# Kernel optimization log

Hardware: AMD Instinct MI355X
Metric: run time of the kernel (lower is better)

Reference implementation:

```python
import jax, jax.numpy as jnp
import numpy as np

B, T, D = 4, 2048, 1024
H = 16
DK = D // H
SCALE = 1.0 / np.sqrt(DK)
EPS_LN = 1e-5
EPS_NORM = 1e-8


def setup_inputs() -> dict:
    key = jax.random.key(0)
    ks = jax.random.split(key, 12)
    gain = 1.0 / np.sqrt(2.0)
    # xavier_uniform bound for square [D, D] weight with gain
    bound = gain * np.sqrt(6.0 / (D + D))

    def w(k):
        return jax.random.uniform(k, (D, D), jnp.float32, -bound, bound)

    return {
        "x": jax.random.normal(ks[0], (B, T, D), jnp.float32),
        "mask": jax.random.bernoulli(ks[1], 0.1, (B, T)),  # True = masked out
        "wq": w(ks[2]), "bq": jnp.zeros((D,), jnp.float32),
        "wk": w(ks[3]), "bk": jnp.zeros((D,), jnp.float32),
        "wv": w(ks[4]), "bv": jnp.zeros((D,), jnp.float32),
        "wo": w(ks[5]), "bo": jnp.zeros((D,), jnp.float32),
        "ln_g": jnp.ones((D,), jnp.float32),
        "ln_b": jnp.zeros((D,), jnp.float32),
    }


def _layernorm(x, g, b):
    mu = jnp.mean(x, axis=-1, keepdims=True)
    var = jnp.var(x, axis=-1, keepdims=True)
    return (x - mu) * jax.lax.rsqrt(var + EPS_LN) * g + b


def _l2norm(x):
    # torch F.normalize: x / clamp_min(||x||_2, eps)
    n = jnp.sqrt(jnp.sum(x * x, axis=-1, keepdims=True))
    return x / jnp.maximum(n, EPS_NORM)


def reference(x, mask, wq, bq, wk, bk, wv, bv, wo, bo, ln_g, ln_b):
    xn = _layernorm(x, ln_g, ln_b)  # q_norm applied to shared input

    def proj(w, bias):
        y = jnp.einsum("btd,ed->bte", xn, w) + bias
        return y.reshape(B, T, H, DK).transpose(0, 2, 1, 3)  # [B,H,T,DK]

    Q = _l2norm(proj(wq, bq))
    K = _l2norm(proj(wk, bk))
    V = proj(wv, bv)

    scores = jnp.einsum("bhqd,bhkd->bhqk", Q, K) * SCALE
    scores = jnp.clip(scores, -10.0, 10.0)
    scores = jnp.where(mask[:, None, None, :], -10000.0, scores)
    scores = scores - jnp.max(scores, axis=-1, keepdims=True)
    attn = jax.nn.softmax(scores, axis=-1)

    out = jnp.einsum("bhqk,bhkd->bhqd", attn, V)
    out = out.transpose(0, 2, 1, 3).reshape(B, T, D)
    out = jnp.einsum("btd,ed->bte", out, wo) + bo
    return out * 0.5
```

## Files before the change

### kernel.cpp

```cpp
#include <hip/hip_runtime.h>
#include <hip/hip_bf16.h>
#include <cstdint>
#include <cstddef>
#include <cstring>

typedef unsigned short u16;
typedef unsigned char u8;
typedef __attribute__((ext_vector_type(8))) short short8;
typedef __attribute__((ext_vector_type(4))) float f32x4;

#define B_    4
#define T_    2048
#define D_    1024
#define H_    16
#define DK_   64
#define QSCALE_ 0.18033688011112042f

__device__ __forceinline__ float bf2f(u16 u) {
    unsigned int x = ((unsigned int)u) << 16;
    float f; __builtin_memcpy(&f, &x, 4); return f;
}
__device__ __forceinline__ u16 f2bf(float f) {
    unsigned int x; __builtin_memcpy(&x, &f, 4);
    x += 0x7fffu + ((x >> 16) & 1u);
    return (u16)(x >> 16);
}
__device__ __forceinline__ unsigned pack_bf16_hu(float lo, float hi) {
    unsigned a, b;
    __builtin_memcpy(&a, &lo, 4);
    __builtin_memcpy(&b, &hi, 4);
    return __builtin_amdgcn_perm(b + 0x8000u, a + 0x8000u, 0x07060302u);
}

__device__ __forceinline__ int sniff_flag(const u16* __restrict__ x, int tid) {
    __shared__ int sc[4];
    int cnt = 0;
    for (int i = tid; i < 512; i += 256) {
        int e = (x[8 * i] >> 7) & 0xFF;
        if (e > 137 || (e >= 1 && e < 97)) cnt++;
    }
    for (int o = 1; o < 64; o <<= 1) cnt += __shfl_xor(cnt, o);
    if ((tid & 63) == 0) sc[tid >> 6] = cnt;
    __syncthreads();
    return (sc[0] + sc[1] + sc[2] + sc[3] > 128) ? 1 : 0;
}

__global__ __launch_bounds__(256) void mega_prep(
    const u16* __restrict__ x, const u8* __restrict__ m,
    const void* wq, const void* wk, const void* wv, const void* wo,
    const void* bq, const void* bk, const void* bv, const void* bo,
    const void* lng, const void* lnb,
    u16* __restrict__ wqc, u16* __restrict__ wkc,
    u16* __restrict__ wvc, u16* __restrict__ woc,
    u16* __restrict__ vecs, float* __restrict__ msk, int* flag,
    u16* __restrict__ xn)
{
    int tid = threadIdx.x;
    int f = sniff_flag(x, tid);
    int id = blockIdx.x;

    if (id < 4096) {
        int mat = id >> 10;
        const void* s = (mat == 0) ? wq : (mat == 1) ? wk : (mat == 2) ? wv : wo;
        u16* d = (mat == 0) ? wqc : (mat == 1) ? wkc : (mat == 2) ? wvc : woc;
        int i4 = (id & 1023) * 256 + tid;
        if (f) {
            float4 v = ((const float4*)s)[i4];
            ushort4 o; o.x = f2bf(v.x); o.y = f2bf(v.y); o.z = f2bf(v.z); o.w = f2bf(v.w);
            ((ushort4*)d)[i4] = o;
        } else {
            ((ushort4*)d)[i4] = ((const ushort4*)s)[i4];
        }
    } else if (id < 12288) {
        __shared__ float rs[4], rq[4];
        int row = id - 4096;
        int t = tid;
        float v[4];
        if (f) {
            float4 f4 = ((const float4*)x)[(size_t)row * 256 + t];
            v[0] = f4.x; v[1] = f4.y; v[2] = f4.z; v[3] = f4.w;
        } else {
            ushort4 uv = ((const ushort4*)x)[(size_t)row * 256 + t];
            v[0] = bf2f(uv.x); v[1] = bf2f(uv.y); v[2] = bf2f(uv.z); v[3] = bf2f(uv.w);
        }
        float s = v[0] + v[1] + v[2] + v[3];
        float q = v[0]*v[0] + v[1]*v[1] + v[2]*v[2] + v[3]*v[3];
        for (int o = 1; o < 64; o <<= 1) { s += __shfl_xor(s, o); q += __shfl_xor(q, o); }
        int wv_ = t >> 6, ln = t & 63;
        if (ln == 0) { rs[wv_] = s; rq[wv_] = q; }
        __syncthreads();
        s = rs[0] + rs[1] + rs[2] + rs[3];
        q = rq[0] + rq[1] + rq[2] + rq[3];
        float mu   = s * (1.0f / D_);
        float var  = q * (1.0f / D_) - mu * mu;
        float rstd = rsqrtf(var + 1e-5f);
        u16 o4[4];
        for (int i = 0; i < 4; i++) {
            float gv, bv_;
            if (f) { gv = ((const float*)lng)[t*4 + i]; bv_ = ((const float*)lnb)[t*4 + i]; }
            else   { gv = bf2f(((const u16*)lng)[t*4 + i]); bv_ = bf2f(((const u16*)lnb)[t*4 + i]); }
            o4[i] = f2bf((v[i] - mu) * rstd * gv + bv_);
        }
        ushort4 ov; ov.x = o4[0]; ov.y = o4[1]; ov.z = o4[2]; ov.w = o4[3];
        *(ushort4*)(xn + (size_t)row * D_ + t * 4) = ov;
    } else {
        __shared__ int sb[4];
        int k = id - 12288;
        int bits = 0;
        for (int i = tid; i < B_ * T_; i += 256)
            if (m[i]) bits |= (i & 7);
        for (int o = 1; o < 64; o <<= 1) bits |= __shfl_xor(bits, o);
        if ((tid & 63) == 0) sb[tid >> 6] = bits;
        __syncthreads();
        bits = sb[0] | sb[1] | sb[2] | sb[3];
        int stride = (bits & 1) ? 1 : (bits & 2) ? 2 : (bits & 4) ? 4 : 8;
        for (int i = tid; i < 1024; i += 256) {
            int idx = k * 1024 + i;
            msk[idx] = m[(size_t)idx * stride] ? -200.f : 0.f;
        }
        if (k == 0) {
            if (tid == 0) *flag = f;
            const void* ss[6] = {bq, bk, bv, bo, lng, lnb};
            for (int t = 0; t < 6; t++) {
                const void* s = ss[t];
                for (int i = tid; i < 1024; i += 256)
                    vecs[t * 1024 + i] = f ? f2bf(((const float*)s)[i]) : ((const u16*)s)[i];
            }
        }
    }
}

__global__ __launch_bounds__(256) void gemm_bt(
    const u16* __restrict__ A,
    const u16* __restrict__ W0, const u16* __restrict__ W1, const u16* __restrict__ W2,
    const u16* __restrict__ bias_all, int bias_idx0,
    u16* __restrict__ C0, u16* __restrict__ C1, u16* __restrict__ C2,
    float scale, const int* __restrict__ flag, int use_flag, int qkv_mode)
{
    const int K = 1024, N = 1024;
    const u16* W; const u16* bias; u16* C;
    if (blockIdx.z == 0)      { W = W0; bias = bias_all + (size_t)bias_idx0 * 1024;       C = C0; }
    else if (blockIdx.z == 1) { W = W1; bias = bias_all + (size_t)(bias_idx0 + 1) * 1024; C = C1; }
    else                      { W = W2; bias = bias_all + (size_t)(bias_idx0 + 2) * 1024; C = C2; }

    __shared__ u16 As[128 * 32];
    __shared__ u16 Bs[128 * 32];

    int tid  = threadIdx.x;
    int wave = tid >> 6, lane = tid & 63;
    int wm = wave >> 1, wn = wave & 1;
    int quad = lane >> 4, l16 = lane & 15;
    int bm = blockIdx.x * 128, bn = blockIdx.y * 128;

    f32x4 acc[4][4];
    const f32x4 fz = {0.f, 0.f, 0.f, 0.f};
    for (int i = 0; i < 4; i++) for (int j = 0; j < 4; j++) acc[i][j] = fz;

    int srow = lane >> 2;
    int scol = (lane & 3) * 8;
    const u16* gA0 = A + (size_t)(bm + wave * 32 + srow) * K + scol;
    const u16* gB0 = W + (size_t)(bn + wave * 32 + srow) * K + scol;

    for (int k0 = 0; k0 < K; k0 += 32) {
        for (int i = 0; i < 2; i++) {
            __builtin_amdgcn_global_load_lds(
                (const __attribute__((address_space(1))) void*)(gA0 + (size_t)i * 16 * K + k0),
                (__attribute__((address_space(3))) void*)(As + (wave * 32 + i * 16) * 32),
                16, 0, 0);
            __builtin_amdgcn_global_load_lds(
                (const __attribute__((address_space(1))) void*)(gB0 + (size_t)i * 16 * K + k0),
                (__attribute__((address_space(3))) void*)(Bs + (wave * 32 + i * 16) * 32),
                16, 0, 0);
        }
        __syncthreads();
        short8 a[4], b[4];
        for (int i = 0; i < 4; i++)
            a[i] = *(const short8*)(As + (wm * 64 + i * 16 + l16) * 32 + quad * 8);
        for (int j = 0; j < 4; j++)
            b[j] = *(const short8*)(Bs + (wn * 64 + j * 16 + l16) * 32 + quad * 8);
        for (int i = 0; i < 4; i++)
            for (int j = 0; j < 4; j++)
                acc[i][j] = __builtin_amdgcn_mfma_f32_16x16x32_bf16(a[i], b[j], acc[i][j], 0, 0, 0);
        __syncthreads();
    }

    if (qkv_mode) {
        if (blockIdx.z == 2) {
            for (int j = 0; j < 4; j++) {
                int col = bn + wn * 64 + j * 16 + l16;
                int h = col >> 6, d = col & 63;
                float bi = bf2f(bias[col]);
                for (int i = 0; i < 4; i++) {
                    int row0 = bm + wm * 64 + i * 16 + quad * 4;
                    int bq = row0 >> 11, t0 = row0 & 2047;
                    ushort4 pk;
                    pk.x = f2bf(acc[i][j][0] + bi); pk.y = f2bf(acc[i][j][1] + bi);
                    pk.z = f2bf(acc[i][j][2] + bi); pk.w = f2bf(acc[i][j][3] + bi);
                    *(ushort4*)(C + ((size_t)((bq * 16 + h) * 64 + d)) * 2048 + t0) = pk;
                }
            }
        } else {
            float sc2 = (blockIdx.z == 0) ? QSCALE_ : 1.0f;
            float bi[4];
            for (int j = 0; j < 4; j++) bi[j] = bf2f(bias[bn + wn * 64 + j * 16 + l16]);
            for (int i = 0; i < 4; i++) {
                int row0 = bm + wm * 64 + i * 16 + quad * 4;
                for (int r = 0; r < 4; r++) {
                    float v[4]; float s = 0.f;
                    for (int j = 0; j < 4; j++) { v[j] = acc[i][j][r] + bi[j]; s += v[j] * v[j]; }
                    s += __shfl_xor(s, 1); s += __shfl_xor(s, 2);
                    s += __shfl_xor(s, 4); s += __shfl_xor(s, 8);
                    float scl = sc2 / fmaxf(sqrtf(s), 1e-8f);
                    for (int j = 0; j < 4; j++) {
                        int col = bn + wn * 64 + j * 16 + l16;
                        C[(size_t)(row0 + r) * N + col] = f2bf(v[j] * scl);
                    }
                }
            }
        }
        return;
    }

    int f32out = use_flag ? *flag : 0;
    for (int j = 0; j < 4; j++) {
        int col = bn + wn * 64 + j * 16 + l16;
        float bi = bf2f(bias[col]);
        for (int i = 0; i < 4; i++) {
            int row0 = bm + wm * 64 + i * 16 + quad * 4;
            for (int r = 0; r < 4; r++) {
                float o = (acc[i][j][r] + bi) * scale;
                if (f32out) ((float*)C)[(size_t)(row0 + r) * N + col] = o;
                else        C[(size_t)(row0 + r) * N + col] = f2bf(o);
            }
        }
    }
}

__global__ __launch_bounds__(256, 4) void attn_kernel(
    const u16* __restrict__ Q, const u16* __restrict__ Kg,
    const u16* __restrict__ Vt, const float* __restrict__ msk,
    u16* __restrict__ Oout)
{
    __shared__ __align__(16) u16 Ks[2 * 64 * 64];
    __shared__ __align__(16) u16 VTs[2 * 64 * 64];

    int tid  = threadIdx.x;
    int wave = tid >> 6, lane = tid & 63;
    int quad = lane >> 4, l16 = lane & 15;
    int q0 = blockIdx.y * 128;
    int b  = blockIdx.x >> 4, h = blockIdx.x & 15;
    const size_t base  = (size_t)b * T_ * D_ + h * DK_;
    const size_t vbase = (size_t)((b * 16 + h) * 64) * T_;

    short8 qa[2][2];
    for (int g = 0; g < 2; g++) {
        const u16* qrow = Q + base + (size_t)(q0 + wave * 32 + g * 16 + l16) * D_;
        qa[g][0] = *(const short8*)(qrow + quad * 8);
        qa[g][1] = *(const short8*)(qrow + 32 + quad * 8);
    }

    const float* mq = msk + b * T_ + quad * 8;

    int rL0 = wave * 8 + (lane >> 3);
    int rL1 = rL0 + 32;
    int c   = lane & 7;
    int k0i = (rL0 & 32) + ((rL0 >> 2) & 3) * 8 + ((rL0 >> 4) & 1) * 4 + (rL0 & 3);
    int k1i = (rL1 & 32) + ((rL1 >> 2) & 3) * 8 + ((rL1 >> 4) & 1) * 4 + (rL1 & 3);
    const u16* kgs0 = Kg + base + (size_t)k0i * D_ + (c ^ (rL0 & 7)) * 8;
    const u16* kgs1 = Kg + base + (size_t)k1i * D_ + (c ^ (rL1 & 7)) * 8;
    const u16* vgs0 = Vt + vbase + (size_t)rL0 * T_ + (c ^ (rL0 & 7)) * 8;
    const u16* vgs1 = Vt + vbase + (size_t)rL1 * T_ + (c ^ (rL1 & 7)) * 8;
    u16* kd0 = Ks  + (wave * 8) * 64;
    u16* kd1 = Ks  + (wave * 8 + 32) * 64;
    u16* vd0 = VTs + (wave * 8) * 64;
    u16* vd1 = VTs + (wave * 8 + 32) * 64;

#define STAGE(BUF, KOFF) do {                                                   \
    __builtin_amdgcn_global_load_lds(                                           \
        (const __attribute__((address_space(1))) void*)(kgs0 + (size_t)(KOFF) * D_), \
        (__attribute__((address_space(3))) void*)(kd0 + (BUF) * 4096), 16, 0, 0); \
    __builtin_amdgcn_global_load_lds(                                           \
        (const __attribute__((address_space(1))) void*)(kgs1 + (size_t)(KOFF) * D_), \
        (__attribute__((address_space(3))) void*)(kd1 + (BUF) * 4096), 16, 0, 0); \
    __builtin_amdgcn_global_load_lds(                                           \
        (const __attribute__((address_space(1))) void*)(vgs0 + (KOFF)),         \
        (__attribute__((address_space(3))) void*)(vd0 + (BUF) * 4096), 16, 0, 0); \
    __builtin_amdgcn_global_load_lds(                                           \
        (const __attribute__((address_space(1))) void*)(vgs1 + (KOFF)),         \
        (__attribute__((address_space(3))) void*)(vd1 + (BUF) * 4096), 16, 0, 0); \
} while (0)

    STAGE(0, 0);
    __syncthreads();

    const u16* kr_lo = Ks + l16 * 64 + ((quad ^ (l16 & 7)) * 8);
    const u16* kr_hi = Ks + l16 * 64 + (((4 + quad) ^ (l16 & 7)) * 8);
    const u16* vr0 = VTs + l16 * 64 + ((quad ^ (l16 & 7)) * 8);
    const u16* vr1 = VTs + l16 * 64 + (((4 + quad) ^ (l16 & 7)) * 8);

    f32x4 o_acc[2][4];
    for (int g = 0; g < 2; g++) for (int j = 0; j < 4; j++) o_acc[g][j] = f32x4{0.f, 0.f, 0.f, 0.f};
    float rowsum[2] = {0.f, 0.f};

#define TILE_BODY(CUR, NXT, KT) do {                                            \
    int ktn = ((KT) + 64) & (T_ - 1);                                           \
    STAGE(NXT, ktn);                                                            \
    f32x4 pmt[2][2];                                                            \
    for (int j2 = 0; j2 < 2; j2++)                                              \
        for (int s = 0; s < 2; s++)                                             \
            pmt[j2][s] = *(const f32x4*)(mq + (KT) + j2 * 32 + s * 4);          \
    __builtin_amdgcn_s_setprio(1);                                              \
    for (int j2 = 0; j2 < 2; j2++) {                                            \
        unsigned pw[2][4];                                                      \
        for (int s = 0; s < 2; s++) {                                           \
            short8 kb0 = *(const short8*)(kr_lo + (CUR) * 4096 + (j2 * 32 + s * 16) * 64); \
            short8 kb1 = *(const short8*)(kr_hi + (CUR) * 4096 + (j2 * 32 + s * 16) * 64); \
            for (int g = 0; g < 2; g++) {                                       \
                f32x4 s4 = __builtin_amdgcn_mfma_f32_16x16x32_bf16(kb0, qa[g][0], pmt[j2][s], 0, 0, 0); \
                s4       = __builtin_amdgcn_mfma_f32_16x16x32_bf16(kb1, qa[g][1], s4, 0, 0, 0); \
                float p0 = __builtin_exp2f(s4[0]);                              \
                float p1 = __builtin_exp2f(s4[1]);                              \
                float p2 = __builtin_exp2f(s4[2]);                              \
                float p3 = __builtin_exp2f(s4[3]);                              \
                rowsum[g] += (p0 + p1) + (p2 + p3);                             \
                pw[g][s * 2]     = pack_bf16_hu(p0, p1);                        \
                pw[g][s * 2 + 1] = pack_bf16_hu(p2, p3);                        \
            }                                                                   \
        }                                                                       \
        short8 pb[2];                                                           \
        __builtin_memcpy(&pb[0], &pw[0][0], 16);                                \
        __builtin_memcpy(&pb[1], &pw[1][0], 16);                                \
        const u16* vr = (j2 ? vr1 : vr0) + (CUR) * 4096;                        \
        for (int jd = 0; jd < 4; jd++) {                                        \
            short8 vv = *(const short8*)(vr + jd * 16 * 64);                    \
            o_acc[0][jd] = __builtin_amdgcn_mfma_f32_16x16x32_bf16(vv, pb[0], o_acc[0][jd], 0, 0, 0); \
            o_acc[1][jd] = __builtin_amdgcn_mfma_f32_16x16x32_bf16(vv, pb[1], o_acc[1][jd], 0, 0, 0); \
        }                                                                       \
    }                                                                           \
    __builtin_amdgcn_s_setprio(0);                                              \
    __syncthreads();                                                            \
} while (0)

    for (int kt = 0; kt < T_; kt += 128) {
        TILE_BODY(0, 1, kt);
        TILE_BODY(1, 0, kt + 64);
    }
#undef TILE_BODY
#undef STAGE

    for (int g = 0; g < 2; g++) {
        float l = rowsum[g];
        l += __shfl_xor(l, 16);
        l += __shfl_xor(l, 32);
        float inv = 1.0f / fmaxf(l, 1e-20f);
        size_t orow = base + (size_t)(q0 + wave * 32 + g * 16 + l16) * D_;
        for (int jd = 0; jd < 4; jd++) {
            ushort4 pk;
            pk.x = f2bf(o_acc[g][jd][0] * inv);
            pk.y = f2bf(o_acc[g][jd][1] * inv);
            pk.z = f2bf(o_acc[g][jd][2] * inv);
            pk.w = f2bf(o_acc[g][jd][3] * inv);
            *(ushort4*)(Oout + orow + jd * 16 + quad * 4) = pk;
        }
    }
}

extern "C" void kernel_launch(void* const* d_in, const int* in_sizes, int n_in,
                              void* d_out, int out_size, void* d_ws, size_t ws_size,
                              hipStream_t stream)
{
    const void* x    = d_in[0];
    const u8*   mask = (const u8*)d_in[1];
    const void* wq   = d_in[2];
    const void* bq   = d_in[3];
    const void* wk   = d_in[4];
    const void* bk   = d_in[5];
    const void* wv   = d_in[6];
    const void* bv   = d_in[7];
    const void* wo   = d_in[8];
    const void* bo   = d_in[9];
    const void* lng  = d_in[10];
    const void* lnb  = d_in[11];

    const size_t NTOK = (size_t)B_ * T_;
    u16* xn  = (u16*)d_ws;
    u16* Kb  = xn + NTOK * D_;
    u16* Vtb = Kb + NTOK * D_;
    u16* wqc = Vtb + NTOK * D_;
    u16* wkc = wqc + (size_t)D_ * D_;
    u16* wvc = wkc + (size_t)D_ * D_;
    u16* woc = wvc + (size_t)D_ * D_;
    u16* vecs = woc + (size_t)D_ * D_;
    float* msk = (float*)(vecs + 6 * 1024);
    int* flag = (int*)(msk + 8192);
    u16* Qb  = (u16*)d_out;

    mega_prep<<<dim3(12296), 256, 0, stream>>>(
        (const u16*)x, mask, wq, wk, wv, wo, bq, bk, bv, bo, lng, lnb,
        wqc, wkc, wvc, woc, vecs, msk, flag, xn);
    gemm_bt<<<dim3(64, 8, 3), 256, 0, stream>>>(xn, wqc, wkc, wvc, vecs, 0, Qb, Kb, Vtb, 1.0f, flag, 0, 1);
    attn_kernel<<<dim3(64, 16), 256, 0, stream>>>(Qb, Kb, Vtb, msk, xn);
    gemm_bt<<<dim3(64, 8, 1), 256, 0, stream>>>(xn, woc, woc, woc, vecs, 3, (u16*)d_out, (u16*)d_out, (u16*)d_out, 0.5f, flag, 1, 0);
}
```

Baseline: 344.7 us.

## Swap GEMM MFMA operands for row-contiguous stores; compute attention rowsum via MFMA

In the GEMM kernel, the MFMA operands are swapped for the Q/K and output projections, so each lane holds four consecutive columns of one row. This allows vectorized ushort4/float4 stores and a two-shuffle L2-norm reduction, replacing strided scalar stores and a four-shuffle reduction. In the attention kernel, the per-row softmax denominator is now accumulated with an extra MFMA against a vector of bf16 ones instead of scalar VALU adds and final shuffles. This adds two MFMAs per sub-tile and sums the bf16-rounded probabilities, which matches the values fed to P·V.

```diff
diff --git a/kernel.cpp b/kernel.cpp
--- a/kernel.cpp
+++ b/kernel.cpp
@@ -152,6 +152,8 @@
     int quad = lane >> 4, l16 = lane & 15;
     int bm = blockIdx.x * 128, bn = blockIdx.y * 128;
 
+    int do_swap = !(qkv_mode && blockIdx.z == 2);
+
     f32x4 acc[4][4];
     const f32x4 fz = {0.f, 0.f, 0.f, 0.f};
     for (int i = 0; i < 4; i++) for (int j = 0; j < 4; j++) acc[i][j] = fz;
@@ -178,59 +180,81 @@
             a[i] = *(const short8*)(As + (wm * 64 + i * 16 + l16) * 32 + quad * 8);
         for (int j = 0; j < 4; j++)
             b[j] = *(const short8*)(Bs + (wn * 64 + j * 16 + l16) * 32 + quad * 8);
-        for (int i = 0; i < 4; i++)
-            for (int j = 0; j < 4; j++)
-                acc[i][j] = __builtin_amdgcn_mfma_f32_16x16x32_bf16(a[i], b[j], acc[i][j], 0, 0, 0);
+        if (do_swap) {
+            for (int i = 0; i < 4; i++)
+                for (int j = 0; j < 4; j++)
+                    acc[i][j] = __builtin_amdgcn_mfma_f32_16x16x32_bf16(b[j], a[i], acc[i][j], 0, 0, 0);
+        } else {
+            for (int i = 0; i < 4; i++)
+                for (int j = 0; j < 4; j++)
+                    acc[i][j] = __builtin_amdgcn_mfma_f32_16x16x32_bf16(a[i], b[j], acc[i][j], 0, 0, 0);
+        }
         __syncthreads();
     }
 
-    if (qkv_mode) {
-        if (blockIdx.z == 2) {
-            for (int j = 0; j < 4; j++) {
-                int col = bn + wn * 64 + j * 16 + l16;
-                int h = col >> 6, d = col & 63;
-                float bi = bf2f(bias[col]);
-                for (int i = 0; i < 4; i++) {
-                    int row0 = bm + wm * 64 + i * 16 + quad * 4;
-                    int bq = row0 >> 11, t0 = row0 & 2047;
-                    ushort4 pk;
-                    pk.x = f2bf(acc[i][j][0] + bi); pk.y = f2bf(acc[i][j][1] + bi);
-                    pk.z = f2bf(acc[i][j][2] + bi); pk.w = f2bf(acc[i][j][3] + bi);
-                    *(ushort4*)(C + ((size_t)((bq * 16 + h) * 64 + d)) * 2048 + t0) = pk;
-                }
-            }
-        } else {
-            float sc2 = (blockIdx.z == 0) ? QSCALE_ : 1.0f;
-            float bi[4];
-            for (int j = 0; j < 4; j++) bi[j] = bf2f(bias[bn + wn * 64 + j * 16 + l16]);
+    if (qkv_mode && blockIdx.z == 2) {
+        for (int j = 0; j < 4; j++) {
+            int col = bn + wn * 64 + j * 16 + l16;
+            int h = col >> 6, d = col & 63;
+            float bi = bf2f(bias[col]);
             for (int i = 0; i < 4; i++) {
                 int row0 = bm + wm * 64 + i * 16 + quad * 4;
+                int bq = row0 >> 11, t0 = row0 & 2047;
+                ushort4 pk;
+                pk.x = f2bf(acc[i][j][0] + bi); pk.y = f2bf(acc[i][j][1] + bi);
+                pk.z = f2bf(acc[i][j][2] + bi); pk.w = f2bf(acc[i][j][3] + bi);
+                *(ushort4*)(C + ((size_t)((bq * 16 + h) * 64 + d)) * 2048 + t0) = pk;
+            }
+        }
+        return;
+    }
+
+    float bi[4][4];
+    for (int j = 0; j < 4; j++) {
+        ushort4 b4 = *(const ushort4*)(bias + bn + wn * 64 + j * 16 + quad * 4);
+        bi[j][0] = bf2f(b4.x); bi[j][1] = bf2f(b4.y);
+        bi[j][2] = bf2f(b4.z); bi[j][3] = bf2f(b4.w);
+    }
+
+    if (qkv_mode) {
+        float sc2 = (blockIdx.z == 0) ? QSCALE_ : 1.0f;
+        for (int i = 0; i < 4; i++) {
+            int row = bm + wm * 64 + i * 16 + l16;
+            float v[4][4]; float s = 0.f;
+            for (int j = 0; j < 4; j++)
                 for (int r = 0; r < 4; r++) {
-                    float v[4]; float s = 0.f;
-                    for (int j = 0; j < 4; j++) { v[j] = acc[i][j][r] + bi[j]; s += v[j] * v[j]; }
-                    s += __shfl_xor(s, 1); s += __shfl_xor(s, 2);
-                    s += __shfl_xor(s, 4); s += __shfl_xor(s, 8);
-                    float scl = sc2 / fmaxf(sqrtf(s), 1e-8f);
-                    for (int j = 0; j < 4; j++) {
-                        int col = bn + wn * 64 + j * 16 + l16;
-                        C[(size_t)(row0 + r) * N + col] = f2bf(v[j] * scl);
-                    }
+                    float val = acc[i][j][r] + bi[j][r];
+                    v[j][r] = val; s += val * val;
                 }
+            s += __shfl_xor(s, 16);
+            s += __shfl_xor(s, 32);
+            float scl = sc2 / fmaxf(sqrtf(s), 1e-8f);
+            for (int j = 0; j < 4; j++) {
+                ushort4 pk;
+                pk.x = f2bf(v[j][0] * scl); pk.y = f2bf(v[j][1] * scl);
+                pk.z = f2bf(v[j][2] * scl); pk.w = f2bf(v[j][3] * scl);
+                *(ushort4*)(C + (size_t)row * N + bn + wn * 64 + j * 16 + quad * 4) = pk;
             }
         }
         return;
     }
 
     int f32out = use_flag ? *flag : 0;
-    for (int j = 0; j < 4; j++) {
-        int col = bn + wn * 64 + j * 16 + l16;
-        float bi = bf2f(bias[col]);
-        for (int i = 0; i < 4; i++) {
-            int row0 = bm + wm * 64 + i * 16 + quad * 4;
-            for (int r = 0; r < 4; r++) {
-                float o = (acc[i][j][r] + bi) * scale;
-                if (f32out) ((float*)C)[(size_t)(row0 + r) * N + col] = o;
-                else        C[(size_t)(row0 + r) * N + col] = f2bf(o);
+    for (int i = 0; i < 4; i++) {
+        int row = bm + wm * 64 + i * 16 + l16;
+        for (int j = 0; j < 4; j++) {
+            int colb = bn + wn * 64 + j * 16 + quad * 4;
+            float o0 = (acc[i][j][0] + bi[j][0]) * scale;
+            float o1 = (acc[i][j][1] + bi[j][1]) * scale;
+            float o2 = (acc[i][j][2] + bi[j][2]) * scale;
+            float o3 = (acc[i][j][3] + bi[j][3]) * scale;
+            if (f32out) {
+                float4 f4 = {o0, o1, o2, o3};
+                *(float4*)(&((float*)C)[(size_t)row * N + colb]) = f4;
+            } else {
+                ushort4 pk;
+                pk.x = f2bf(o0); pk.y = f2bf(o1); pk.z = f2bf(o2); pk.w = f2bf(o3);
+                *(ushort4*)(C + (size_t)row * N + colb) = pk;
             }
         }
     }
@@ -300,7 +324,9 @@
 
     f32x4 o_acc[2][4];
     for (int g = 0; g < 2; g++) for (int j = 0; j < 4; j++) o_acc[g][j] = f32x4{0.f, 0.f, 0.f, 0.f};
-    float rowsum[2] = {0.f, 0.f};
+    f32x4 rs_acc[2] = {f32x4{0.f,0.f,0.f,0.f}, f32x4{0.f,0.f,0.f,0.f}};
+    const short8 vone = {(short)0x3F80, (short)0x3F80, (short)0x3F80, (short)0x3F80,
+                         (short)0x3F80, (short)0x3F80, (short)0x3F80, (short)0x3F80};
 
 #define TILE_BODY(CUR, NXT, KT) do {                                            \
     int ktn = ((KT) + 64) & (T_ - 1);                                           \
@@ -322,7 +348,6 @@
                 float p1 = __builtin_exp2f(s4[1]);                              \
                 float p2 = __builtin_exp2f(s4[2]);                              \
                 float p3 = __builtin_exp2f(s4[3]);                              \
-                rowsum[g] += (p0 + p1) + (p2 + p3);                             \
                 pw[g][s * 2]     = pack_bf16_hu(p0, p1);                        \
                 pw[g][s * 2 + 1] = pack_bf16_hu(p2, p3);                        \
             }                                                                   \
@@ -330,6 +355,8 @@
         short8 pb[2];                                                           \
         __builtin_memcpy(&pb[0], &pw[0][0], 16);                                \
         __builtin_memcpy(&pb[1], &pw[1][0], 16);                                \
+        rs_acc[0] = __builtin_amdgcn_mfma_f32_16x16x32_bf16(vone, pb[0], rs_acc[0], 0, 0, 0); \
+        rs_acc[1] = __builtin_amdgcn_mfma_f32_16x16x32_bf16(vone, pb[1], rs_acc[1], 0, 0, 0); \
         const u16* vr = (j2 ? vr1 : vr0) + (CUR) * 4096;                        \
         for (int jd = 0; jd < 4; jd++) {                                        \
             short8 vv = *(const short8*)(vr + jd * 16 * 64);                    \
@@ -349,10 +376,7 @@
 #undef STAGE
 
     for (int g = 0; g < 2; g++) {
-        float l = rowsum[g];
-        l += __shfl_xor(l, 16);
-        l += __shfl_xor(l, 32);
-        float inv = 1.0f / fmaxf(l, 1e-20f);
+        float inv = 1.0f / fmaxf(rs_acc[g][0], 1e-20f);
         size_t orow = base + (size_t)(q0 + wave * 32 + g * 16 + l16) * D_;
         for (int jd = 0; jd < 4; jd++) {
             ushort4 pk;
```

Result: slower. 366.2 us (+6.2%).
